# Kernel tuning notes

Measured on AMD Instinct MI355X. Metric: run time of the kernel, lower is better.

## Reference

```python
import jax, jax.numpy as jnp
from jax import lax
import numpy as np

K_TOP = 100
NMS_THRESH = 0.5
SUBJECT_CATEGORY_ID = 0


def box_cxcywh_to_xyxy(b):
    cx, cy, w, h = b[..., 0], b[..., 1], b[..., 2], b[..., 3]
    return jnp.stack([cx - 0.5 * w, cy - 0.5 * h, cx + 0.5 * w, cy + 0.5 * h], axis=-1)


def _pairwise_iou(boxes):
    # boxes: [K,4] xyxy; uses the +1 pixel convention from the original numpy NMS
    x1, y1, x2, y2 = boxes[:, 0], boxes[:, 1], boxes[:, 2], boxes[:, 3]
    area = (x2 - x1 + 1.0) * (y2 - y1 + 1.0)
    xx1 = jnp.maximum(x1[:, None], x1[None, :])
    yy1 = jnp.maximum(y1[:, None], y1[None, :])
    xx2 = jnp.minimum(x2[:, None], x2[None, :])
    yy2 = jnp.minimum(y2[:, None], y2[None, :])
    w = jnp.maximum(0.0, xx2 - xx1 + 1.0)
    h = jnp.maximum(0.0, yy2 - yy1 + 1.0)
    inter = w * h
    union = area[:, None] + area[None, :] - inter
    return inter / union


def _nms_keep(sub_boxes, obj_boxes, obj_labels, hoi_scores):
    # Greedy grouped pairwise NMS for one image.
    # Grouping key degenerates to object label (subject cat and verb-row are constant).
    K = sub_boxes.shape[0]
    max_scores = hoi_scores.max(axis=-1)
    order = jnp.argsort(-max_scores)
    ovr = _pairwise_iou(sub_boxes) * _pairwise_iou(obj_boxes)  # [K,K]
    same_group = obj_labels[:, None] == obj_labels[None, :]
    ovr = jnp.where(same_group, ovr, 0.0)
    ovr_s = ovr[order][:, order]
    upper = jnp.triu(jnp.ones((K, K), dtype=bool), k=1)
    sup_mat = (ovr_s > NMS_THRESH) & upper  # suppression only of later (lower-score) items

    def body(i, st):
        suppressed, keep = st
        ki = jnp.logical_not(suppressed[i])
        keep = keep.at[i].set(ki)
        suppressed = suppressed | (ki & sup_mat[i])
        return suppressed, keep

    _, keep_sorted = lax.fori_loop(0, K, body, (jnp.zeros(K, bool), jnp.zeros(K, bool)))
    return jnp.zeros(K, bool).at[order].set(keep_sorted)


def setup_inputs() -> dict:
    key = jax.random.key(0)
    k1, k2, k3, k4, k5, k6 = jax.random.split(key, 6)
    B, Q, C, V = 256, 300, 81, 117
    return {
        "pred_obj_logits": jax.random.normal(k1, (B, Q, C), dtype=jnp.float32),
        "pred_verb_logits": jax.random.normal(k2, (B, Q, V), dtype=jnp.float32),
        "pred_sub_boxes": jax.random.uniform(k3, (B, Q, 4), dtype=jnp.float32),
        "pred_obj_boxes": jax.random.uniform(k4, (B, Q, 4), dtype=jnp.float32),
        "correct_mat": (jax.random.uniform(k5, (V, C), dtype=jnp.float32) > 0.3).astype(jnp.float32),
        "target_sizes": jax.random.randint(k6, (B, 2), 200, 640, dtype=jnp.int32),
    }


def reference(pred_obj_logits, pred_verb_logits, pred_sub_boxes, pred_obj_boxes, correct_mat, target_sizes):
    B, Q, C = pred_obj_logits.shape
    V = pred_verb_logits.shape[-1]

    obj_prob = jax.nn.softmax(pred_obj_logits, axis=-1)       # [B,Q,C]  (no_obj=False)
    verb_scores = jax.nn.sigmoid(pred_verb_logits)            # [B,Q,V]

    topk_values, topk_indexes = lax.top_k(obj_prob.reshape(B, Q * C), K_TOP)  # [B,100]
    topk_boxes = topk_indexes // C
    obj_labels = topk_indexes % C

    vs = jnp.take_along_axis(verb_scores, topk_boxes[..., None], axis=1)      # [B,100,V]
    ob = jnp.take_along_axis(pred_obj_boxes, topk_boxes[..., None], axis=1)   # [B,100,4]
    sb = jnp.take_along_axis(pred_sub_boxes, topk_boxes[..., None], axis=1)

    img_h = target_sizes[:, 0].astype(jnp.float32)
    img_w = target_sizes[:, 1].astype(jnp.float32)
    scale_fct = jnp.stack([img_w, img_h, img_w, img_h], axis=1)  # [B,4]
    sub_boxes = box_cxcywh_to_xyxy(sb) * scale_fct[:, None, :]
    obj_boxes = box_cxcywh_to_xyxy(ob) * scale_fct[:, None, :]

    hoi_scores = vs * topk_values[..., None]                    # [B,100,V]
    # masks[b,k,v] = correct_mat[v, obj_labels[b,k]]
    masks = correct_mat.T[obj_labels]                           # [B,100,V]
    hoi_scores = hoi_scores * masks

    keep = jax.vmap(_nms_keep)(sub_boxes, obj_boxes, obj_labels, hoi_scores)  # [B,100] bool
    final_scores = hoi_scores * keep[..., None].astype(hoi_scores.dtype)

    return final_scores, topk_values, obj_labels, sub_boxes, obj_boxes, keep
```

## Files before the change

### kernel.cpp

```cpp
#include <hip/hip_runtime.h>
#include <cmath>

#pragma clang fp contract(off)

#define NT 1024
constexpr int B_ = 256, Q_ = 300, C_ = 81, V_ = 117, K_ = 100;
constexpr int QC_ = Q_ * C_;
constexpr int KV_ = K_ * V_;
constexpr int NB  = 2048;
constexpr int CAP = 1024;

using u32 = unsigned int;
using u64 = unsigned long long;
using u16 = unsigned short;
using u8  = unsigned char;

constexpr int OFF_P16  = 0;
constexpr int OFF_HIST = 48600;
constexpr int OFF_RMAX = OFF_HIST + 8192;
constexpr int OFF_RINV = OFF_RMAX + 1200;
constexpr int OFF_BSUB = OFF_RINV + 1200;
constexpr int OFF_BOBJ = OFF_BSUB + 1600;
constexpr int OFF_SUPR = OFF_BOBJ + 1600;
constexpr int OFF_SELV = OFF_SUPR + 1600;
constexpr int OFF_SELI = OFF_SELV + 400;
constexpr int OFF_MAXB = OFF_SELI + 400;
constexpr int OFF_ORD  = OFF_MAXB + 400;
constexpr int OFF_MISC = OFF_ORD + 104;
constexpr int SMEM_SZ  = OFF_MISC + 48;
static_assert(SMEM_SZ <= 65536, "LDS overflow");

__device__ __forceinline__ u64 shfl_xor_u64(u64 v, int mask) {
    u32 lo = (u32)v, hi = (u32)(v >> 32);
    lo = (u32)__shfl_xor((int)lo, mask, 64);
    hi = (u32)__shfl_xor((int)hi, mask, 64);
    return ((u64)hi << 32) | lo;
}

__device__ __forceinline__ float iou1(const float* a, const float* b) {
    float areaA = (a[2] - a[0] + 1.f) * (a[3] - a[1] + 1.f);
    float areaB = (b[2] - b[0] + 1.f) * (b[3] - b[1] + 1.f);
    float xx1 = fmaxf(a[0], b[0]);
    float yy1 = fmaxf(a[1], b[1]);
    float xx2 = fminf(a[2], b[2]);
    float yy2 = fminf(a[3], b[3]);
    float w = fmaxf(0.f, xx2 - xx1 + 1.f);
    float h = fmaxf(0.f, yy2 - yy1 + 1.f);
    float inter = w * h;
    return inter / (areaA + areaB - inter);
}

__global__ __launch_bounds__(NT) void hoi_kernel(
    const float* __restrict__ obj_logits,
    const float* __restrict__ verb_logits,
    const float* __restrict__ sub_boxes_in,
    const float* __restrict__ obj_boxes_in,
    const float* __restrict__ cm,
    const int*   __restrict__ tsizes,
    float* __restrict__ out)
{
    const int b = blockIdx.x;
    const int tid = threadIdx.x;

    __shared__ __align__(16) u8 smem[SMEM_SZ];
    u16*   p16     = (u16*)(smem + OFF_P16);
    float* hs      = (float*)(smem + OFF_P16);
    u32*   hist    = (u32*)(smem + OFF_HIST);
    u64*   cand    = (u64*)(smem + OFF_HIST);
    float* rowmax  = (float*)(smem + OFF_RMAX);
    float* rinv    = (float*)(smem + OFF_RINV);
    float (*bsub)[4]   = (float(*)[4])(smem + OFF_BSUB);
    float (*bobj)[4]   = (float(*)[4])(smem + OFF_BOBJ);
    u32   (*suprow)[4] = (u32(*)[4])(smem + OFF_SUPR);
    float* sel_val = (float*)(smem + OFF_SELV);
    u32*   sel_idx = (u32*)(smem + OFF_SELI);
    u32*   maxbits = (u32*)(smem + OFF_MAXB);
    u8*    order8  = (u8*)(smem + OFF_ORD);
    u32*   skeep     = (u32*)(smem + OFF_MISC);
    u32*   keep_bits = (u32*)(smem + OFF_MISC + 16);
    u32*   s_cnt     = (u32*)(smem + OFF_MISC + 32);
    int*   sT        = (int*)(smem + OFF_MISC + 36);
    int*   sW        = (int*)(smem + OFF_MISC + 40);
    u32*   sAcc      = (u32*)(smem + OFF_MISC + 44);
    u32*   swsum   = (u32*)(smem + OFF_BSUB);
    u64*   wred    = (u64*)(smem + OFF_BOBJ);
    u64*   s_prev  = (u64*)(smem + OFF_SUPR);

    const float* lg = obj_logits + (size_t)b * QC_;

    for (int i = tid; i < NB; i += NT) hist[i] = 0;
    if (tid == 0) *s_cnt = 0;
    __syncthreads();

    {
        int g = tid >> 5, l = tid & 31;
        bool have2 = (l < C_ - 64);
        for (int q = g; q < Q_; q += 32) {
            const float* row = lg + q * C_;
            float v0 = row[l], v1 = row[l + 32];
            float v2 = have2 ? row[l + 64] : -INFINITY;
            float m = fmaxf(fmaxf(v0, v1), v2);
            for (int off = 16; off; off >>= 1) m = fmaxf(m, __shfl_xor(m, off, 64));
            float e0 = expf(v0 - m), e1 = expf(v1 - m);
            float e2 = have2 ? expf(v2 - m) : 0.f;
            float s = e0 + e1 + e2;
            for (int off = 16; off; off >>= 1) s += __shfl_xor(s, off, 64);
            float ri = 1.f / s;
            float p0 = e0 * ri, p1 = e1 * ri;
            u32 b0 = __float_as_uint(p0), b1 = __float_as_uint(p1);
            p16[q * C_ + l]      = (u16)(b0 >> 16);
            p16[q * C_ + l + 32] = (u16)(b1 >> 16);
            atomicAdd(&hist[b0 >> 21], 1u);
            atomicAdd(&hist[b1 >> 21], 1u);
            if (have2) {
                float p2 = e2 * ri;
                u32 b2 = __float_as_uint(p2);
                p16[q * C_ + l + 64] = (u16)(b2 >> 16);
                atomicAdd(&hist[b2 >> 21], 1u);
            }
            if (l == 0) { rowmax[q] = m; rinv[q] = ri; }
        }
    }
    __syncthreads();

    u32 my_c, my_suf;
    {
        int t = tid;
        my_c = hist[2 * t] + hist[2 * t + 1];
        my_suf = my_c;
        #pragma unroll
        for (int off = 1; off < 64; off <<= 1) {
            u32 o = (u32)__shfl_down((int)my_suf, off, 64);
            my_suf += ((tid & 63) + off < 64) ? o : 0;
        }
        if ((tid & 63) == 0) swsum[tid >> 6] = my_suf;
    }
    __syncthreads();
    if (tid < 16) {
        u32 sufW = swsum[tid];
        #pragma unroll
        for (int off = 1; off < 16; off <<= 1) {
            u32 o = (u32)__shfl_down((int)sufW, off, 64);
            sufW += (tid + off < 16) ? o : 0;
        }
        u32 nxt = (u32)__shfl_down((int)sufW, 1, 64);
        if (tid == 15) nxt = 0;
        if (sufW >= (u32)K_ && nxt < (u32)K_) { *sW = tid; *sAcc = nxt; }
    }
    __syncthreads();
    if ((tid >> 6) == *sW) {
        u32 above = *sAcc + (my_suf - my_c);
        if (above < (u32)K_ && above + my_c >= (u32)K_) {
            u32 acc = above + hist[2 * tid + 1];
            *sT = (acc >= (u32)K_) ? (2 * tid + 1) : (2 * tid);
        }
    }
    __syncthreads();
    const int T = *sT;
    __syncthreads();

    for (int i = tid; i < QC_; i += NT) {
        u32 pb = p16[i];
        if ((int)(pb >> 5) >= T) {
            u32 pos = atomicAdd(s_cnt, 1u);
            if (pos < (u32)CAP) {
                int q = i / C_;
                float p = expf(lg[i] - rowmax[q]) * rinv[q];
                cand[pos] = ((u64)__float_as_uint(p) << 32) | (u32)(~i);
            }
        }
    }
    __syncthreads();
    const int ncand = (int)*s_cnt;

    auto cswap = [](u64& a, u64& bb, bool up) {
        if ((a > bb) == up) { u64 t = a; a = bb; bb = t; }
    };

    if (ncand <= 256) {
        if (tid < 64) {
            u64 v0 = (tid < ncand) ? cand[tid] : 0ull;
            u64 v1 = (64 + tid < ncand) ? cand[64 + tid] : 0ull;
            u64 v2 = (128 + tid < ncand) ? cand[128 + tid] : 0ull;
            u64 v3 = (192 + tid < ncand) ? cand[192 + tid] : 0ull;
            for (int k = 2; k <= 256; k <<= 1) {
                for (int j = k >> 1; j > 0; j >>= 1) {
                    if (j == 128) {
                        cswap(v0, v2, true);
                        cswap(v1, v3, true);
                    } else if (j == 64) {
                        cswap(v0, v1, true);
                        cswap(v2, v3, (k == 256));
                    } else {
                        auto step = [&](u64& v, int ebase) {
                            u64 pv = shfl_xor_u64(v, j);
                            int e = ebase + tid;
                            bool up = ((e & k) == 0);
                            bool lower = ((e & j) == 0);
                            u64 mn = v < pv ? v : pv;
                            u64 mx = v < pv ? pv : v;
                            v = (lower == up) ? mn : mx;
                        };
                        step(v0, 0); step(v1, 64); step(v2, 128); step(v3, 192);
                    }
                }
            }
            int e2 = 128 + tid;
            if (e2 >= 156) {
                int t = 255 - e2;
                sel_val[t] = __uint_as_float((u32)(v2 >> 32));
                sel_idx[t] = ~(u32)v2;
            }
            int t3 = 255 - (192 + tid);
            sel_val[t3] = __uint_as_float((u32)(v3 >> 32));
            sel_idx[t3] = ~(u32)v3;
        }
    } else if (ncand <= CAP) {
        for (int e = tid; e < CAP; e += NT)
            if (e >= ncand) cand[e] = 0;
        __syncthreads();
        for (int k = 2; k <= CAP; k <<= 1) {
            for (int j = k >> 1; j > 0; j >>= 1) {
                int e = tid, partner = e ^ j;
                if (partner > e) {
                    u64 a = cand[e], bb = cand[partner];
                    bool up = ((e & k) == 0);
                    if ((a > bb) == up) { cand[e] = bb; cand[partner] = a; }
                }
                __syncthreads();
            }
        }
        if (tid < K_) {
            u64 m = cand[CAP - 1 - tid];
            sel_val[tid] = __uint_as_float((u32)(m >> 32));
            sel_idx[tid] = ~(u32)m;
        }
    } else {
        if (tid == 0) *s_prev = ~0ull;
        __syncthreads();
        for (int r = 0; r < K_; r++) {
            u64 prev = *s_prev;
            u64 local = 0;
            for (int i = tid; i < QC_; i += NT) {
                int q = i / C_;
                float p = expf(lg[i] - rowmax[q]) * rinv[q];
                u64 key = ((u64)__float_as_uint(p) << 32) | (u32)(~i);
                if (key < prev && key > local) local = key;
            }
            for (int off = 32; off > 0; off >>= 1) {
                u64 o = shfl_xor_u64(local, off);
                if (o > local) local = o;
            }
            if ((tid & 63) == 0) wred[tid >> 6] = local;
            __syncthreads();
            if (tid == 0) {
                u64 m = wred[0];
                for (int wv = 1; wv < 16; wv++) if (wred[wv] > m) m = wred[wv];
                *s_prev = m;
                u32 idx = ~(u32)m;
                if (idx >= (u32)QC_) idx = 0;
                sel_val[r] = __uint_as_float((u32)(m >> 32));
                sel_idx[r] = idx;
            }
            __syncthreads();
        }
    }
    __syncthreads();

    if (tid < K_) {
        int idx = (int)sel_idx[tid];
        int q = idx / C_;
        float iw = (float)tsizes[b * 2 + 1];
        float ih = (float)tsizes[b * 2 + 0];
        float4 sb = ((const float4*)sub_boxes_in)[(size_t)b * Q_ + q];
        float4 ob = ((const float4*)obj_boxes_in)[(size_t)b * Q_ + q];
        bsub[tid][0] = (sb.x - 0.5f * sb.z) * iw; bsub[tid][1] = (sb.y - 0.5f * sb.w) * ih;
        bsub[tid][2] = (sb.x + 0.5f * sb.z) * iw; bsub[tid][3] = (sb.y + 0.5f * sb.w) * ih;
        bobj[tid][0] = (ob.x - 0.5f * ob.z) * iw; bobj[tid][1] = (ob.y - 0.5f * ob.w) * ih;
        bobj[tid][2] = (ob.x + 0.5f * ob.z) * iw; bobj[tid][3] = (ob.y + 0.5f * ob.w) * ih;
        suprow[tid][0] = 0; suprow[tid][1] = 0; suprow[tid][2] = 0; suprow[tid][3] = 0;
    }
    if (tid >= 128 && tid < 132) keep_bits[tid - 128] = 0;
    __syncthreads();

    for (int f = tid; f < KV_; f += NT) {
        int r = f / V_, v = f - r * V_;
        int idx = (int)sel_idx[r];
        int q = idx / C_, lab = idx - q * C_;
        float x = verb_logits[((size_t)b * Q_ + q) * V_ + v];
        float s = 1.f / (1.f + expf(-x));
        hs[f] = s * sel_val[r] * cm[v * C_ + lab];
    }
    __syncthreads();

    if (tid < 800) {
        int r = tid >> 3, j = tid & 7;
        float m = 0.f;
        for (int k = 0; k < 15; k++) {
            int v = j * 15 + k;
            if (v < V_) m = fmaxf(m, hs[r * V_ + v]);
        }
        for (int off = 4; off; off >>= 1) m = fmaxf(m, __shfl_xor(m, off, 64));
        if (j == 0) maxbits[r] = __float_as_uint(m);
    }
    __syncthreads();

    if (tid < 800) {
        int r = tid >> 3, j = tid & 7;
        u64 kr = ((u64)maxbits[r] << 32) | (u32)(~r);
        int rank = 0;
        for (int k = 0; k < 13; k++) {
            int jj = j * 13 + k;
            if (jj < K_) {
                u64 kj = ((u64)maxbits[jj] << 32) | (u32)(~jj);
                rank += (kj > kr) ? 1 : 0;
            }
        }
        for (int off = 4; off; off >>= 1) rank += __shfl_xor(rank, off, 64);
        if (j == 0) order8[rank] = (u8)r;
    }
    __syncthreads();

    for (int e = tid; e < K_ * K_; e += NT) {
        int i = e / K_, j = e - i * K_;
        if (j > i) {
            int ri = order8[i], rj = order8[j];
            u32 li = sel_idx[ri] % (u32)C_, lj = sel_idx[rj] % (u32)C_;
            if (li == lj) {
                float o = iou1(bsub[ri], bsub[rj]) * iou1(bobj[ri], bobj[rj]);
                if (o > 0.5f)
                    atomicOr(&suprow[i][j >> 5], 1u << (j & 31));
            }
        }
    }
    __syncthreads();

    if (tid < 64) {
        u32 ra0 = suprow[tid][0], ra1 = suprow[tid][1], ra2 = suprow[tid][2], ra3 = suprow[tid][3];
        u32 rb0 = 0, rb1 = 0, rb2 = 0, rb3 = 0;
        if (tid < K_ - 64) {
            rb0 = suprow[tid + 64][0]; rb1 = suprow[tid + 64][1];
            rb2 = suprow[tid + 64][2]; rb3 = suprow[tid + 64][3];
        }
        u32 acc[4] = {0, 0, 0, 0};
        u32 km[4]  = {0, 0, 0, 0};
        #pragma unroll
        for (int i = 0; i < K_; i++) {
            u32 r0, r1, r2, r3;
            if (i < 64) {
                r0 = (u32)__shfl((int)ra0, i, 64); r1 = (u32)__shfl((int)ra1, i, 64);
                r2 = (u32)__shfl((int)ra2, i, 64); r3 = (u32)__shfl((int)ra3, i, 64);
            } else {
                r0 = (u32)__shfl((int)rb0, i - 64, 64); r1 = (u32)__shfl((int)rb1, i - 64, 64);
                r2 = (u32)__shfl((int)rb2, i - 64, 64); r3 = (u32)__shfl((int)rb3, i - 64, 64);
            }
            bool sup_i = (acc[i >> 5] >> (i & 31)) & 1u;
            if (!sup_i) {
                km[i >> 5] |= 1u << (i & 31);
                acc[0] |= r0; acc[1] |= r1; acc[2] |= r2; acc[3] |= r3;
            }
        }
        if (tid == 0) { skeep[0] = km[0]; skeep[1] = km[1]; skeep[2] = km[2]; skeep[3] = km[3]; }
    }
    __syncthreads();
    if (tid < K_) {
        if ((skeep[tid >> 5] >> (tid & 31)) & 1u) {
            int r = order8[tid];
            atomicOr(&keep_bits[r >> 5], 1u << (r & 31));
        }
    }
    __syncthreads();

    float* o0 = out;
    float* o1 = out + (size_t)B_ * KV_;
    float* o2 = o1 + (size_t)B_ * K_;
    float* o3 = o2 + (size_t)B_ * K_;
    float* o4 = o3 + (size_t)B_ * K_ * 4;
    float* o5 = o4 + (size_t)B_ * K_ * 4;

    for (int f = tid; f < KV_; f += NT) {
        int r = f / V_;
        bool kp = (keep_bits[r >> 5] >> (r & 31)) & 1u;
        o0[(size_t)b * KV_ + f] = kp ? hs[f] : 0.f;
    }
    if (tid < K_) {
        bool kp = (keep_bits[tid >> 5] >> (tid & 31)) & 1u;
        o1[(size_t)b * K_ + tid] = sel_val[tid];
        o2[(size_t)b * K_ + tid] = (float)(sel_idx[tid] % (u32)C_);
        o5[(size_t)b * K_ + tid] = kp ? 1.f : 0.f;
    }
    if (tid < K_ * 4) {
        int r = tid >> 2, k = tid & 3;
        o3[((size_t)b * K_) * 4 + tid] = bsub[r][k];
        o4[((size_t)b * K_) * 4 + tid] = bobj[r][k];
    }
}

extern "C" void kernel_launch(void* const* d_in, const int* in_sizes, int n_in,
                              void* d_out, int out_size, void* d_ws, size_t ws_size,
                              hipStream_t stream) {
    const float* obj_logits  = (const float*)d_in[0];
    const float* verb_logits = (const float*)d_in[1];
    const float* sub_boxes   = (const float*)d_in[2];
    const float* obj_boxes   = (const float*)d_in[3];
    const float* cm          = (const float*)d_in[4];
    const int*   ts          = (const int*)d_in[5];
    hipLaunchKernelGGL(hoi_kernel, dim3(B_), dim3(NT), 0, stream,
                       obj_logits, verb_logits, sub_boxes, obj_boxes, cm, ts,
                       (float*)d_out);
}
```

Before: 143.1 us.

## Split per-image top-k into partitioned select kernel and merge/finish kernel

Splits each image's 300 query rows into 8 partitions, each handled by its own 256-thread block. Each block computes the softmax, builds a finer 8192-bin histogram, and writes its local top-128 candidates to workspace. A second kernel merges the 1024 candidates per image with a bitonic sort and then runs the verb scoring, NMS and output stages. The aim is far more blocks than the 256 images provide, better GPU occupancy for the softmax/top-k stage, and no recompute of exps. In exchange it adds a second launch, a workspace round trip, and a switch to the fast __expf.

```diff
diff --git a/kernel.cpp b/kernel.cpp
--- a/kernel.cpp
+++ b/kernel.cpp
@@ -2,33 +2,24 @@
 #include <cmath>
 
 #pragma clang fp contract(off)
-
-#define NT 1024
-constexpr int B_ = 256, Q_ = 300, C_ = 81, V_ = 117, K_ = 100;
-constexpr int QC_ = Q_ * C_;
-constexpr int KV_ = K_ * V_;
-constexpr int NB  = 2048;
-constexpr int CAP = 1024;
 
 using u32 = unsigned int;
 using u64 = unsigned long long;
 using u16 = unsigned short;
 using u8  = unsigned char;
 
-constexpr int OFF_P16  = 0;
-constexpr int OFF_HIST = 48600;
-constexpr int OFF_RMAX = OFF_HIST + 8192;
-constexpr int OFF_RINV = OFF_RMAX + 1200;
-constexpr int OFF_BSUB = OFF_RINV + 1200;
-constexpr int OFF_BOBJ = OFF_BSUB + 1600;
-constexpr int OFF_SUPR = OFF_BOBJ + 1600;
-constexpr int OFF_SELV = OFF_SUPR + 1600;
-constexpr int OFF_SELI = OFF_SELV + 400;
-constexpr int OFF_MAXB = OFF_SELI + 400;
-constexpr int OFF_ORD  = OFF_MAXB + 400;
-constexpr int OFF_MISC = OFF_ORD + 104;
-constexpr int SMEM_SZ  = OFF_MISC + 48;
-static_assert(SMEM_SZ <= 65536, "LDS overflow");
+constexpr int B_ = 256, Q_ = 300, C_ = 81, V_ = 117, K_ = 100;
+constexpr int QC_ = Q_ * C_;
+constexpr int KV_ = K_ * V_;
+
+constexpr int PARTS = 8;
+constexpr int RPP   = 38;
+constexpr int TOPP  = 128;
+constexpr int K1T   = 256;
+constexpr int NB1   = 8192;
+constexpr int CAP   = 1024;
+
+constexpr int K2T   = 1024;
 
 __device__ __forceinline__ u64 shfl_xor_u64(u64 v, int mask) {
     u32 lo = (u32)v, hi = (u32)(v >> 32);
@@ -50,128 +41,115 @@
     return inter / (areaA + areaB - inter);
 }
 
-__global__ __launch_bounds__(NT) void hoi_kernel(
+__global__ __launch_bounds__(K1T) void k1_select(
     const float* __restrict__ obj_logits,
-    const float* __restrict__ verb_logits,
-    const float* __restrict__ sub_boxes_in,
-    const float* __restrict__ obj_boxes_in,
-    const float* __restrict__ cm,
-    const int*   __restrict__ tsizes,
-    float* __restrict__ out)
+    u64* __restrict__ wsc)
 {
-    const int b = blockIdx.x;
+    const int blk = blockIdx.x;
+    const int b = blk >> 3, p = blk & 7;
+    const int row0 = p * RPP;
+    const int nrows = min(RPP, Q_ - row0);
+    const float* lg = obj_logits + (size_t)b * QC_ + (size_t)row0 * C_;
     const int tid = threadIdx.x;
 
-    __shared__ __align__(16) u8 smem[SMEM_SZ];
-    u16*   p16     = (u16*)(smem + OFF_P16);
-    float* hs      = (float*)(smem + OFF_P16);
-    u32*   hist    = (u32*)(smem + OFF_HIST);
-    u64*   cand    = (u64*)(smem + OFF_HIST);
-    float* rowmax  = (float*)(smem + OFF_RMAX);
-    float* rinv    = (float*)(smem + OFF_RINV);
-    float (*bsub)[4]   = (float(*)[4])(smem + OFF_BSUB);
-    float (*bobj)[4]   = (float(*)[4])(smem + OFF_BOBJ);
-    u32   (*suprow)[4] = (u32(*)[4])(smem + OFF_SUPR);
-    float* sel_val = (float*)(smem + OFF_SELV);
-    u32*   sel_idx = (u32*)(smem + OFF_SELI);
-    u32*   maxbits = (u32*)(smem + OFF_MAXB);
-    u8*    order8  = (u8*)(smem + OFF_ORD);
-    u32*   skeep     = (u32*)(smem + OFF_MISC);
-    u32*   keep_bits = (u32*)(smem + OFF_MISC + 16);
-    u32*   s_cnt     = (u32*)(smem + OFF_MISC + 32);
-    int*   sT        = (int*)(smem + OFF_MISC + 36);
-    int*   sW        = (int*)(smem + OFF_MISC + 40);
-    u32*   sAcc      = (u32*)(smem + OFF_MISC + 44);
-    u32*   swsum   = (u32*)(smem + OFF_BSUB);
-    u64*   wred    = (u64*)(smem + OFF_BOBJ);
-    u64*   s_prev  = (u64*)(smem + OFF_SUPR);
-
-    const float* lg = obj_logits + (size_t)b * QC_;
-
-    for (int i = tid; i < NB; i += NT) hist[i] = 0;
+    __shared__ __align__(16) u8 sm[32768 + 64];
+    u32* hist  = (u32*)sm;
+    u64* cand  = (u64*)sm;
+    u32* s_cnt = (u32*)(sm + 32768);
+    int* sT    = (int*)(sm + 32772);
+    u32* swsum = (u32*)(sm + 32776);
+
+    for (int i = tid; i < NB1; i += K1T) hist[i] = 0;
     if (tid == 0) *s_cnt = 0;
     __syncthreads();
 
-    {
-        int g = tid >> 5, l = tid & 31;
-        bool have2 = (l < C_ - 64);
-        for (int q = g; q < Q_; q += 32) {
-            const float* row = lg + q * C_;
+    const int g = tid >> 5, l = tid & 31;
+    const bool have2 = (l < C_ - 64);
+    u32 pb0[5], pb1[5], pb2[5];
+    #pragma unroll
+    for (int it = 0; it < 5; it++) {
+        int r = g + (it << 3);
+        if (r < nrows) {
+            const float* row = lg + r * C_;
             float v0 = row[l], v1 = row[l + 32];
             float v2 = have2 ? row[l + 64] : -INFINITY;
             float m = fmaxf(fmaxf(v0, v1), v2);
             for (int off = 16; off; off >>= 1) m = fmaxf(m, __shfl_xor(m, off, 64));
-            float e0 = expf(v0 - m), e1 = expf(v1 - m);
-            float e2 = have2 ? expf(v2 - m) : 0.f;
+            float e0 = __expf(v0 - m), e1 = __expf(v1 - m);
+            float e2 = have2 ? __expf(v2 - m) : 0.f;
             float s = e0 + e1 + e2;
             for (int off = 16; off; off >>= 1) s += __shfl_xor(s, off, 64);
             float ri = 1.f / s;
-            float p0 = e0 * ri, p1 = e1 * ri;
-            u32 b0 = __float_as_uint(p0), b1 = __float_as_uint(p1);
-            p16[q * C_ + l]      = (u16)(b0 >> 16);
-            p16[q * C_ + l + 32] = (u16)(b1 >> 16);
-            atomicAdd(&hist[b0 >> 21], 1u);
-            atomicAdd(&hist[b1 >> 21], 1u);
+            u32 b0 = __float_as_uint(e0 * ri), b1 = __float_as_uint(e1 * ri);
+            pb0[it] = b0; pb1[it] = b1;
+            atomicAdd(&hist[b0 >> 19], 1u);
+            atomicAdd(&hist[b1 >> 19], 1u);
             if (have2) {
-                float p2 = e2 * ri;
-                u32 b2 = __float_as_uint(p2);
-                p16[q * C_ + l + 64] = (u16)(b2 >> 16);
-                atomicAdd(&hist[b2 >> 21], 1u);
-            }
-            if (l == 0) { rowmax[q] = m; rinv[q] = ri; }
-        }
-    }
-    __syncthreads();
-
-    u32 my_c, my_suf;
+                u32 b2 = __float_as_uint(e2 * ri);
+                pb2[it] = b2;
+                atomicAdd(&hist[b2 >> 19], 1u);
+            }
+        }
+    }
+    __syncthreads();
+
     {
-        int t = tid;
-        my_c = hist[2 * t] + hist[2 * t + 1];
-        my_suf = my_c;
+        u32 c = 0;
+        int base = tid * (NB1 / K1T);
+        for (int k = 0; k < NB1 / K1T; k++) c += hist[base + k];
+        u32 suf = c;
         #pragma unroll
         for (int off = 1; off < 64; off <<= 1) {
-            u32 o = (u32)__shfl_down((int)my_suf, off, 64);
-            my_suf += ((tid & 63) + off < 64) ? o : 0;
-        }
-        if ((tid & 63) == 0) swsum[tid >> 6] = my_suf;
-    }
-    __syncthreads();
-    if (tid < 16) {
-        u32 sufW = swsum[tid];
-        #pragma unroll
-        for (int off = 1; off < 16; off <<= 1) {
-            u32 o = (u32)__shfl_down((int)sufW, off, 64);
-            sufW += (tid + off < 16) ? o : 0;
-        }
-        u32 nxt = (u32)__shfl_down((int)sufW, 1, 64);
-        if (tid == 15) nxt = 0;
-        if (sufW >= (u32)K_ && nxt < (u32)K_) { *sW = tid; *sAcc = nxt; }
-    }
-    __syncthreads();
-    if ((tid >> 6) == *sW) {
-        u32 above = *sAcc + (my_suf - my_c);
-        if (above < (u32)K_ && above + my_c >= (u32)K_) {
-            u32 acc = above + hist[2 * tid + 1];
-            *sT = (acc >= (u32)K_) ? (2 * tid + 1) : (2 * tid);
+            u32 o = (u32)__shfl_down((int)suf, off, 64);
+            suf += ((tid & 63) + off < 64) ? o : 0;
+        }
+        if ((tid & 63) == 0) swsum[tid >> 6] = suf;
+        __syncthreads();
+        u32 aw = 0;
+        for (int w = (tid >> 6) + 1; w < 4; w++) aw += swsum[w];
+        u32 above = aw + (suf - c);
+        if (above < (u32)TOPP && above + c >= (u32)TOPP) {
+            u32 acc = above;
+            for (int bn = base + NB1 / K1T - 1; bn >= base; bn--) {
+                u32 h = hist[bn];
+                if (acc + h >= (u32)TOPP) { *sT = bn; break; }
+                acc += h;
+            }
         }
     }
     __syncthreads();
     const int T = *sT;
     __syncthreads();
 
-    for (int i = tid; i < QC_; i += NT) {
-        u32 pb = p16[i];
-        if ((int)(pb >> 5) >= T) {
-            u32 pos = atomicAdd(s_cnt, 1u);
-            if (pos < (u32)CAP) {
-                int q = i / C_;
-                float p = expf(lg[i] - rowmax[q]) * rinv[q];
-                cand[pos] = ((u64)__float_as_uint(p) << 32) | (u32)(~i);
-            }
-        }
-    }
-    __syncthreads();
-    const int ncand = (int)*s_cnt;
+    #pragma unroll
+    for (int it = 0; it < 5; it++) {
+        int r = g + (it << 3);
+        if (r < nrows) {
+            u32 base_i = (u32)((row0 + r) * C_);
+            u32 b0 = pb0[it];
+            if ((int)(b0 >> 19) >= T) {
+                u32 pos = atomicAdd(s_cnt, 1u);
+                if (pos < (u32)CAP) cand[pos] = ((u64)b0 << 32) | (u32)(~(base_i + l));
+            }
+            u32 b1v = pb1[it];
+            if ((int)(b1v >> 19) >= T) {
+                u32 pos = atomicAdd(s_cnt, 1u);
+                if (pos < (u32)CAP) cand[pos] = ((u64)b1v << 32) | (u32)(~(base_i + l + 32));
+            }
+            if (have2) {
+                u32 b2 = pb2[it];
+                if ((int)(b2 >> 19) >= T) {
+                    u32 pos = atomicAdd(s_cnt, 1u);
+                    if (pos < (u32)CAP) cand[pos] = ((u64)b2 << 32) | (u32)(~(base_i + l + 64));
+                }
+            }
+        }
+    }
+    __syncthreads();
+    int ncand = (int)*s_cnt;
+    if (ncand > CAP) ncand = CAP;
+
+    u64* outp = wsc + (size_t)b * (PARTS * TOPP) + p * TOPP;
 
     auto cswap = [](u64& a, u64& bb, bool up) {
         if ((a > bb) == up) { u64 t = a; a = bb; bb = t; }
@@ -205,65 +183,86 @@
                     }
                 }
             }
-            int e2 = 128 + tid;
-            if (e2 >= 156) {
-                int t = 255 - e2;
-                sel_val[t] = __uint_as_float((u32)(v2 >> 32));
-                sel_idx[t] = ~(u32)v2;
-            }
-            int t3 = 255 - (192 + tid);
-            sel_val[t3] = __uint_as_float((u32)(v3 >> 32));
-            sel_idx[t3] = ~(u32)v3;
-        }
-    } else if (ncand <= CAP) {
-        for (int e = tid; e < CAP; e += NT)
+            outp[tid]      = v2;
+            outp[64 + tid] = v3;
+        }
+    } else {
+        for (int e = tid; e < CAP; e += K1T)
             if (e >= ncand) cand[e] = 0;
         __syncthreads();
         for (int k = 2; k <= CAP; k <<= 1) {
             for (int j = k >> 1; j > 0; j >>= 1) {
-                int e = tid, partner = e ^ j;
-                if (partner > e) {
-                    u64 a = cand[e], bb = cand[partner];
-                    bool up = ((e & k) == 0);
-                    if ((a > bb) == up) { cand[e] = bb; cand[partner] = a; }
+                for (int e = tid; e < CAP; e += K1T) {
+                    int partner = e ^ j;
+                    if (partner > e) {
+                        u64 a = cand[e], bb = cand[partner];
+                        bool up = ((e & k) == 0);
+                        if ((a > bb) == up) { cand[e] = bb; cand[partner] = a; }
+                    }
                 }
                 __syncthreads();
             }
         }
-        if (tid < K_) {
-            u64 m = cand[CAP - 1 - tid];
-            sel_val[tid] = __uint_as_float((u32)(m >> 32));
-            sel_idx[tid] = ~(u32)m;
-        }
-    } else {
-        if (tid == 0) *s_prev = ~0ull;
-        __syncthreads();
-        for (int r = 0; r < K_; r++) {
-            u64 prev = *s_prev;
-            u64 local = 0;
-            for (int i = tid; i < QC_; i += NT) {
-                int q = i / C_;
-                float p = expf(lg[i] - rowmax[q]) * rinv[q];
-                u64 key = ((u64)__float_as_uint(p) << 32) | (u32)(~i);
-                if (key < prev && key > local) local = key;
-            }
-            for (int off = 32; off > 0; off >>= 1) {
-                u64 o = shfl_xor_u64(local, off);
-                if (o > local) local = o;
-            }
-            if ((tid & 63) == 0) wred[tid >> 6] = local;
+        if (tid < TOPP) outp[tid] = cand[CAP - 1 - tid];
+    }
+}
+
+constexpr int OFF_HS   = 0;
+constexpr int OFF_BSUB = 46800;
+constexpr int OFF_BOBJ = OFF_BSUB + 1600;
+constexpr int OFF_SUPR = OFF_BOBJ + 1600;
+constexpr int OFF_SELV = OFF_SUPR + 1600;
+constexpr int OFF_SELI = OFF_SELV + 400;
+constexpr int OFF_MAXB = OFF_SELI + 400;
+constexpr int OFF_ORD  = OFF_MAXB + 400;
+constexpr int OFF_MISC = OFF_ORD + 104;
+constexpr int SMEM2    = OFF_MISC + 32;
+static_assert(SMEM2 <= 65536, "LDS overflow");
+
+__global__ __launch_bounds__(K2T) void k2_finish(
+    const u64*  __restrict__ wsc,
+    const float* __restrict__ verb_logits,
+    const float* __restrict__ sub_boxes_in,
+    const float* __restrict__ obj_boxes_in,
+    const float* __restrict__ cm,
+    const int*   __restrict__ tsizes,
+    float* __restrict__ out)
+{
+    const int b = blockIdx.x;
+    const int tid = threadIdx.x;
+
+    __shared__ __align__(16) u8 smem[SMEM2];
+    u64*   cand    = (u64*)(smem + OFF_HS);
+    float* hs      = (float*)(smem + OFF_HS);
+    float (*bsub)[4]   = (float(*)[4])(smem + OFF_BSUB);
+    float (*bobj)[4]   = (float(*)[4])(smem + OFF_BOBJ);
+    u32   (*suprow)[4] = (u32(*)[4])(smem + OFF_SUPR);
+    float* sel_val = (float*)(smem + OFF_SELV);
+    u32*   sel_idx = (u32*)(smem + OFF_SELI);
+    u32*   maxbits = (u32*)(smem + OFF_MAXB);
+    u8*    order8  = (u8*)(smem + OFF_ORD);
+    u32*   skeep     = (u32*)(smem + OFF_MISC);
+    u32*   keep_bits = (u32*)(smem + OFF_MISC + 16);
+
+    cand[tid] = wsc[(size_t)b * (PARTS * TOPP) + tid];
+    __syncthreads();
+    for (int k = 2; k <= CAP; k <<= 1) {
+        for (int j = k >> 1; j > 0; j >>= 1) {
+            int e = tid, partner = e ^ j;
+            if (partner > e) {
+                u64 a = cand[e], bb = cand[partner];
+                bool up = ((e & k) == 0);
+                if ((a > bb) == up) { cand[e] = bb; cand[partner] = a; }
+            }
             __syncthreads();
-            if (tid == 0) {
-                u64 m = wred[0];
-                for (int wv = 1; wv < 16; wv++) if (wred[wv] > m) m = wred[wv];
-                *s_prev = m;
-                u32 idx = ~(u32)m;
-                if (idx >= (u32)QC_) idx = 0;
-                sel_val[r] = __uint_as_float((u32)(m >> 32));
-                sel_idx[r] = idx;
-            }
-            __syncthreads();
-        }
+        }
+    }
+    if (tid < K_) {
+        u64 m = cand[CAP - 1 - tid];
+        u32 idx = ~(u32)m;
+        if (idx >= (u32)QC_) idx = 0;
+        sel_val[tid] = __uint_as_float((u32)(m >> 32));
+        sel_idx[tid] = idx;
     }
     __syncthreads();
 
@@ -283,12 +282,12 @@
     if (tid >= 128 && tid < 132) keep_bits[tid - 128] = 0;
     __syncthreads();
 
-    for (int f = tid; f < KV_; f += NT) {
+    for (int f = tid; f < KV_; f += K2T) {
         int r = f / V_, v = f - r * V_;
         int idx = (int)sel_idx[r];
         int q = idx / C_, lab = idx - q * C_;
         float x = verb_logits[((size_t)b * Q_ + q) * V_ + v];
-        float s = 1.f / (1.f + expf(-x));
+        float s = 1.f / (1.f + __expf(-x));
         hs[f] = s * sel_val[r] * cm[v * C_ + lab];
     }
     __syncthreads();
@@ -321,7 +320,7 @@
     }
     __syncthreads();
 
-    for (int e = tid; e < K_ * K_; e += NT) {
+    for (int e = tid; e < K_ * K_; e += K2T) {
         int i = e / K_, j = e - i * K_;
         if (j > i) {
             int ri = order8[i], rj = order8[j];
@@ -378,7 +377,7 @@
     float* o4 = o3 + (size_t)B_ * K_ * 4;
     float* o5 = o4 + (size_t)B_ * K_ * 4;
 
-    for (int f = tid; f < KV_; f += NT) {
+    for (int f = tid; f < KV_; f += K2T) {
         int r = f / V_;
         bool kp = (keep_bits[r >> 5] >> (r & 31)) & 1u;
         o0[(size_t)b * KV_ + f] = kp ? hs[f] : 0.f;
@@ -405,7 +404,11 @@
     const float* obj_boxes   = (const float*)d_in[3];
     const float* cm          = (const float*)d_in[4];
     const int*   ts          = (const int*)d_in[5];
-    hipLaunchKernelGGL(hoi_kernel, dim3(B_), dim3(NT), 0, stream,
-                       obj_logits, verb_logits, sub_boxes, obj_boxes, cm, ts,
+    u64* wsc = (u64*)d_ws;
+
+    hipLaunchKernelGGL(k1_select, dim3(B_ * PARTS), dim3(K1T), 0, stream,
+                       obj_logits, wsc);
+    hipLaunchKernelGGL(k2_finish, dim3(B_), dim3(K2T), 0, stream,
+                       wsc, verb_logits, sub_boxes, obj_boxes, cm, ts,
                        (float*)d_out);
 }
```

New measurement: 180.2 us. +25.9%, slower.

## Split top-k selection across two half-image blocks and merge in a second kernel

Applied to the files above, without the earlier changes.

Splits the per-image kernel in two. The first kernel runs two blocks per image, each covering half the queries and keeping a local top-128 in workspace. The second kernel merges the two sorted halves with a bitonic merge and then does scoring and NMS. This doubles the parallelism of the softmax/histogram/select stage, which was limited to 256 blocks, and also swaps expf for __expf. The costs are an extra launch, a global workspace round trip, and possible precision differences from __expf. The fallback for more than 1024 candidates is dropped (it now clamps), which could change results in degenerate cases.

```diff
diff --git a/kernel.cpp b/kernel.cpp
--- a/kernel.cpp
+++ b/kernel.cpp
@@ -9,26 +9,14 @@
 constexpr int KV_ = K_ * V_;
 constexpr int NB  = 2048;
 constexpr int CAP = 1024;
+constexpr int HROWS = 150;
+constexpr int HQC   = HROWS * C_;
+constexpr int TOPH  = 128;
 
 using u32 = unsigned int;
 using u64 = unsigned long long;
 using u16 = unsigned short;
 using u8  = unsigned char;
-
-constexpr int OFF_P16  = 0;
-constexpr int OFF_HIST = 48600;
-constexpr int OFF_RMAX = OFF_HIST + 8192;
-constexpr int OFF_RINV = OFF_RMAX + 1200;
-constexpr int OFF_BSUB = OFF_RINV + 1200;
-constexpr int OFF_BOBJ = OFF_BSUB + 1600;
-constexpr int OFF_SUPR = OFF_BOBJ + 1600;
-constexpr int OFF_SELV = OFF_SUPR + 1600;
-constexpr int OFF_SELI = OFF_SELV + 400;
-constexpr int OFF_MAXB = OFF_SELI + 400;
-constexpr int OFF_ORD  = OFF_MAXB + 400;
-constexpr int OFF_MISC = OFF_ORD + 104;
-constexpr int SMEM_SZ  = OFF_MISC + 48;
-static_assert(SMEM_SZ <= 65536, "LDS overflow");
 
 __device__ __forceinline__ u64 shfl_xor_u64(u64 v, int mask) {
     u32 lo = (u32)v, hi = (u32)(v >> 32);
@@ -50,43 +38,36 @@
     return inter / (areaA + areaB - inter);
 }
 
-__global__ __launch_bounds__(NT) void hoi_kernel(
+constexpr int OFF1_P16  = 0;
+constexpr int OFF1_HIST = 24304;
+constexpr int OFF1_RMAX = OFF1_HIST + 8192;
+constexpr int OFF1_RINV = OFF1_RMAX + 608;
+constexpr int OFF1_SW   = OFF1_RINV + 608;
+constexpr int OFF1_MISC = OFF1_SW + 64;
+constexpr int SMEM1     = OFF1_MISC + 16;
+static_assert(SMEM1 <= 65536, "K1 LDS overflow");
+
+__global__ __launch_bounds__(NT, 8) void k1_select(
     const float* __restrict__ obj_logits,
-    const float* __restrict__ verb_logits,
-    const float* __restrict__ sub_boxes_in,
-    const float* __restrict__ obj_boxes_in,
-    const float* __restrict__ cm,
-    const int*   __restrict__ tsizes,
-    float* __restrict__ out)
+    u64* __restrict__ wsc)
 {
-    const int b = blockIdx.x;
+    const int blk = blockIdx.x;
+    const int b = blk >> 1, h = blk & 1;
+    const int row0 = h * HROWS;
+    const float* lg = obj_logits + (size_t)b * QC_ + (size_t)row0 * C_;
     const int tid = threadIdx.x;
 
-    __shared__ __align__(16) u8 smem[SMEM_SZ];
-    u16*   p16     = (u16*)(smem + OFF_P16);
-    float* hs      = (float*)(smem + OFF_P16);
-    u32*   hist    = (u32*)(smem + OFF_HIST);
-    u64*   cand    = (u64*)(smem + OFF_HIST);
-    float* rowmax  = (float*)(smem + OFF_RMAX);
-    float* rinv    = (float*)(smem + OFF_RINV);
-    float (*bsub)[4]   = (float(*)[4])(smem + OFF_BSUB);
-    float (*bobj)[4]   = (float(*)[4])(smem + OFF_BOBJ);
-    u32   (*suprow)[4] = (u32(*)[4])(smem + OFF_SUPR);
-    float* sel_val = (float*)(smem + OFF_SELV);
-    u32*   sel_idx = (u32*)(smem + OFF_SELI);
-    u32*   maxbits = (u32*)(smem + OFF_MAXB);
-    u8*    order8  = (u8*)(smem + OFF_ORD);
-    u32*   skeep     = (u32*)(smem + OFF_MISC);
-    u32*   keep_bits = (u32*)(smem + OFF_MISC + 16);
-    u32*   s_cnt     = (u32*)(smem + OFF_MISC + 32);
-    int*   sT        = (int*)(smem + OFF_MISC + 36);
-    int*   sW        = (int*)(smem + OFF_MISC + 40);
-    u32*   sAcc      = (u32*)(smem + OFF_MISC + 44);
-    u32*   swsum   = (u32*)(smem + OFF_BSUB);
-    u64*   wred    = (u64*)(smem + OFF_BOBJ);
-    u64*   s_prev  = (u64*)(smem + OFF_SUPR);
-
-    const float* lg = obj_logits + (size_t)b * QC_;
+    __shared__ __align__(16) u8 sm[SMEM1];
+    u16*   p16    = (u16*)(sm + OFF1_P16);
+    u32*   hist   = (u32*)(sm + OFF1_HIST);
+    u64*   cand   = (u64*)(sm + OFF1_HIST);
+    float* rowmax = (float*)(sm + OFF1_RMAX);
+    float* rinv   = (float*)(sm + OFF1_RINV);
+    u32*   swsum  = (u32*)(sm + OFF1_SW);
+    u32*   s_cnt  = (u32*)(sm + OFF1_MISC);
+    int*   sT     = (int*)(sm + OFF1_MISC + 4);
+    int*   sW     = (int*)(sm + OFF1_MISC + 8);
+    u32*   sAcc   = (u32*)(sm + OFF1_MISC + 12);
 
     for (int i = tid; i < NB; i += NT) hist[i] = 0;
     if (tid == 0) *s_cnt = 0;
@@ -95,26 +76,24 @@
     {
         int g = tid >> 5, l = tid & 31;
         bool have2 = (l < C_ - 64);
-        for (int q = g; q < Q_; q += 32) {
+        for (int q = g; q < HROWS; q += 32) {
             const float* row = lg + q * C_;
             float v0 = row[l], v1 = row[l + 32];
             float v2 = have2 ? row[l + 64] : -INFINITY;
             float m = fmaxf(fmaxf(v0, v1), v2);
             for (int off = 16; off; off >>= 1) m = fmaxf(m, __shfl_xor(m, off, 64));
-            float e0 = expf(v0 - m), e1 = expf(v1 - m);
-            float e2 = have2 ? expf(v2 - m) : 0.f;
+            float e0 = __expf(v0 - m), e1 = __expf(v1 - m);
+            float e2 = have2 ? __expf(v2 - m) : 0.f;
             float s = e0 + e1 + e2;
             for (int off = 16; off; off >>= 1) s += __shfl_xor(s, off, 64);
             float ri = 1.f / s;
-            float p0 = e0 * ri, p1 = e1 * ri;
-            u32 b0 = __float_as_uint(p0), b1 = __float_as_uint(p1);
+            u32 b0 = __float_as_uint(e0 * ri), b1 = __float_as_uint(e1 * ri);
             p16[q * C_ + l]      = (u16)(b0 >> 16);
             p16[q * C_ + l + 32] = (u16)(b1 >> 16);
             atomicAdd(&hist[b0 >> 21], 1u);
             atomicAdd(&hist[b1 >> 21], 1u);
             if (have2) {
-                float p2 = e2 * ri;
-                u32 b2 = __float_as_uint(p2);
+                u32 b2 = __float_as_uint(e2 * ri);
                 p16[q * C_ + l + 64] = (u16)(b2 >> 16);
                 atomicAdd(&hist[b2 >> 21], 1u);
             }
@@ -125,8 +104,7 @@
 
     u32 my_c, my_suf;
     {
-        int t = tid;
-        my_c = hist[2 * t] + hist[2 * t + 1];
+        my_c = hist[2 * tid] + hist[2 * tid + 1];
         my_suf = my_c;
         #pragma unroll
         for (int off = 1; off < 64; off <<= 1) {
@@ -145,33 +123,36 @@
         }
         u32 nxt = (u32)__shfl_down((int)sufW, 1, 64);
         if (tid == 15) nxt = 0;
-        if (sufW >= (u32)K_ && nxt < (u32)K_) { *sW = tid; *sAcc = nxt; }
+        if (sufW >= (u32)TOPH && nxt < (u32)TOPH) { *sW = tid; *sAcc = nxt; }
     }
     __syncthreads();
     if ((tid >> 6) == *sW) {
         u32 above = *sAcc + (my_suf - my_c);
-        if (above < (u32)K_ && above + my_c >= (u32)K_) {
+        if (above < (u32)TOPH && above + my_c >= (u32)TOPH) {
             u32 acc = above + hist[2 * tid + 1];
-            *sT = (acc >= (u32)K_) ? (2 * tid + 1) : (2 * tid);
+            *sT = (acc >= (u32)TOPH) ? (2 * tid + 1) : (2 * tid);
         }
     }
     __syncthreads();
     const int T = *sT;
     __syncthreads();
 
-    for (int i = tid; i < QC_; i += NT) {
+    for (int i = tid; i < HQC; i += NT) {
         u32 pb = p16[i];
         if ((int)(pb >> 5) >= T) {
             u32 pos = atomicAdd(s_cnt, 1u);
             if (pos < (u32)CAP) {
                 int q = i / C_;
-                float p = expf(lg[i] - rowmax[q]) * rinv[q];
-                cand[pos] = ((u64)__float_as_uint(p) << 32) | (u32)(~i);
-            }
-        }
-    }
-    __syncthreads();
-    const int ncand = (int)*s_cnt;
+                float p = __expf(lg[i] - rowmax[q]) * rinv[q];
+                cand[pos] = ((u64)__float_as_uint(p) << 32) | (u32)(~(row0 * C_ + i));
+            }
+        }
+    }
+    __syncthreads();
+    int ncand = (int)*s_cnt;
+    if (ncand > CAP) ncand = CAP;
+
+    u64* outp = wsc + (size_t)b * 256 + h * TOPH;
 
     auto cswap = [](u64& a, u64& bb, bool up) {
         if ((a > bb) == up) { u64 t = a; a = bb; bb = t; }
@@ -205,17 +186,10 @@
                     }
                 }
             }
-            int e2 = 128 + tid;
-            if (e2 >= 156) {
-                int t = 255 - e2;
-                sel_val[t] = __uint_as_float((u32)(v2 >> 32));
-                sel_idx[t] = ~(u32)v2;
-            }
-            int t3 = 255 - (192 + tid);
-            sel_val[t3] = __uint_as_float((u32)(v3 >> 32));
-            sel_idx[t3] = ~(u32)v3;
-        }
-    } else if (ncand <= CAP) {
+            outp[tid]      = v2;
+            outp[64 + tid] = v3;
+        }
+    } else {
         for (int e = tid; e < CAP; e += NT)
             if (e >= ncand) cand[e] = 0;
         __syncthreads();
@@ -230,41 +204,80 @@
                 __syncthreads();
             }
         }
-        if (tid < K_) {
-            u64 m = cand[CAP - 1 - tid];
-            sel_val[tid] = __uint_as_float((u32)(m >> 32));
-            sel_idx[tid] = ~(u32)m;
-        }
-    } else {
-        if (tid == 0) *s_prev = ~0ull;
-        __syncthreads();
-        for (int r = 0; r < K_; r++) {
-            u64 prev = *s_prev;
-            u64 local = 0;
-            for (int i = tid; i < QC_; i += NT) {
-                int q = i / C_;
-                float p = expf(lg[i] - rowmax[q]) * rinv[q];
-                u64 key = ((u64)__float_as_uint(p) << 32) | (u32)(~i);
-                if (key < prev && key > local) local = key;
-            }
-            for (int off = 32; off > 0; off >>= 1) {
-                u64 o = shfl_xor_u64(local, off);
-                if (o > local) local = o;
-            }
-            if ((tid & 63) == 0) wred[tid >> 6] = local;
-            __syncthreads();
-            if (tid == 0) {
-                u64 m = wred[0];
-                for (int wv = 1; wv < 16; wv++) if (wred[wv] > m) m = wred[wv];
-                *s_prev = m;
-                u32 idx = ~(u32)m;
-                if (idx >= (u32)QC_) idx = 0;
-                sel_val[r] = __uint_as_float((u32)(m >> 32));
-                sel_idx[r] = idx;
-            }
-            __syncthreads();
-        }
-    }
+        if (tid < TOPH) outp[tid] = cand[CAP - TOPH + tid];
+    }
+}
+
+constexpr int OFF_HS   = 0;
+constexpr int OFF_BSUB = 46800;
+constexpr int OFF_BOBJ = OFF_BSUB + 1600;
+constexpr int OFF_SUPR = OFF_BOBJ + 1600;
+constexpr int OFF_SELV = OFF_SUPR + 1600;
+constexpr int OFF_SELI = OFF_SELV + 400;
+constexpr int OFF_MAXB = OFF_SELI + 400;
+constexpr int OFF_ORD  = OFF_MAXB + 400;
+constexpr int OFF_MISC = OFF_ORD + 104;
+constexpr int SMEM2    = OFF_MISC + 32;
+static_assert(SMEM2 <= 65536, "K2 LDS overflow");
+
+__global__ __launch_bounds__(NT) void k2_finish(
+    const u64*  __restrict__ wsc,
+    const float* __restrict__ verb_logits,
+    const float* __restrict__ sub_boxes_in,
+    const float* __restrict__ obj_boxes_in,
+    const float* __restrict__ cm,
+    const int*   __restrict__ tsizes,
+    float* __restrict__ out)
+{
+    const int b = blockIdx.x;
+    const int tid = threadIdx.x;
+
+    __shared__ __align__(16) u8 smem[SMEM2];
+    float* hs      = (float*)(smem + OFF_HS);
+    float (*bsub)[4]   = (float(*)[4])(smem + OFF_BSUB);
+    float (*bobj)[4]   = (float(*)[4])(smem + OFF_BOBJ);
+    u32   (*suprow)[4] = (u32(*)[4])(smem + OFF_SUPR);
+    float* sel_val = (float*)(smem + OFF_SELV);
+    u32*   sel_idx = (u32*)(smem + OFF_SELI);
+    u32*   maxbits = (u32*)(smem + OFF_MAXB);
+    u8*    order8  = (u8*)(smem + OFF_ORD);
+    u32*   skeep     = (u32*)(smem + OFF_MISC);
+    u32*   keep_bits = (u32*)(smem + OFF_MISC + 16);
+
+    if (tid < 64) {
+        const u64* base = wsc + (size_t)b * 256;
+        u64 v0 = base[tid];
+        u64 v1 = base[64 + tid];
+        u64 v2 = base[255 - tid];
+        u64 v3 = base[191 - tid];
+        auto cswap = [](u64& a, u64& bb) {
+            if (a > bb) { u64 t = a; a = bb; bb = t; }
+        };
+        cswap(v0, v2); cswap(v1, v3);
+        cswap(v0, v1); cswap(v2, v3);
+        for (int j = 32; j > 0; j >>= 1) {
+            auto step = [&](u64& v) {
+                u64 pv = shfl_xor_u64(v, j);
+                bool lower = ((tid & j) == 0);
+                u64 mn = v < pv ? v : pv;
+                u64 mx = v < pv ? pv : v;
+                v = lower ? mn : mx;
+            };
+            step(v0); step(v1); step(v2); step(v3);
+        }
+        int e2 = 128 + tid;
+        if (e2 >= 156) {
+            int t = 255 - e2;
+            u32 idx = ~(u32)v2; if (idx >= (u32)QC_) idx = 0;
+            sel_val[t] = __uint_as_float((u32)(v2 >> 32));
+            sel_idx[t] = idx;
+        }
+        int t3 = 63 - tid;
+        u32 idx3 = ~(u32)v3; if (idx3 >= (u32)QC_) idx3 = 0;
+        sel_val[t3] = __uint_as_float((u32)(v3 >> 32));
+        sel_idx[t3] = idx3;
+    }
+    if (tid >= 128 && tid < 132) keep_bits[tid - 128] = 0;
     __syncthreads();
 
     if (tid < K_) {
@@ -280,7 +293,6 @@
         bobj[tid][2] = (ob.x + 0.5f * ob.z) * iw; bobj[tid][3] = (ob.y + 0.5f * ob.w) * ih;
         suprow[tid][0] = 0; suprow[tid][1] = 0; suprow[tid][2] = 0; suprow[tid][3] = 0;
     }
-    if (tid >= 128 && tid < 132) keep_bits[tid - 128] = 0;
     __syncthreads();
 
     for (int f = tid; f < KV_; f += NT) {
@@ -288,7 +300,7 @@
         int idx = (int)sel_idx[r];
         int q = idx / C_, lab = idx - q * C_;
         float x = verb_logits[((size_t)b * Q_ + q) * V_ + v];
-        float s = 1.f / (1.f + expf(-x));
+        float s = 1.f / (1.f + __expf(-x));
         hs[f] = s * sel_val[r] * cm[v * C_ + lab];
     }
     __syncthreads();
@@ -405,7 +417,11 @@
     const float* obj_boxes   = (const float*)d_in[3];
     const float* cm          = (const float*)d_in[4];
     const int*   ts          = (const int*)d_in[5];
-    hipLaunchKernelGGL(hoi_kernel, dim3(B_), dim3(NT), 0, stream,
-                       obj_logits, verb_logits, sub_boxes, obj_boxes, cm, ts,
+    u64* wsc = (u64*)d_ws;
+
+    hipLaunchKernelGGL(k1_select, dim3(B_ * 2), dim3(NT), 0, stream,
+                       obj_logits, wsc);
+    hipLaunchKernelGGL(k2_finish, dim3(B_), dim3(NT), 0, stream,
+                       wsc, verb_logits, sub_boxes, obj_boxes, cm, ts,
                        (float*)d_out);
 }
```

Result: slower. 146.8 us (+2.6%).

## Write HOI scores directly to global, zero suppressed rows later, use fast exp

Applied to the files above, without the earlier changes.

Computes the per-row verb scores one wavefront per row, writing them straight to the output and computing the row max by a wave shuffle reduction, instead of staging them in shared memory and running a separate max pass. After NMS, only suppressed rows are overwritten with zeros, so the final full copy out of shared memory goes away. All expf calls become __expf. The fast exp can change low-order bits of the probabilities, and the scores written before NMS are global writes that suppressed rows then overwrite a second time.

```diff
diff --git a/kernel.cpp b/kernel.cpp
--- a/kernel.cpp
+++ b/kernel.cpp
@@ -64,7 +64,6 @@
 
     __shared__ __align__(16) u8 smem[SMEM_SZ];
     u16*   p16     = (u16*)(smem + OFF_P16);
-    float* hs      = (float*)(smem + OFF_P16);
     u32*   hist    = (u32*)(smem + OFF_HIST);
     u64*   cand    = (u64*)(smem + OFF_HIST);
     float* rowmax  = (float*)(smem + OFF_RMAX);
@@ -88,6 +87,13 @@
 
     const float* lg = obj_logits + (size_t)b * QC_;
 
+    float* o0 = out;
+    float* o1 = out + (size_t)B_ * KV_;
+    float* o2 = o1 + (size_t)B_ * K_;
+    float* o3 = o2 + (size_t)B_ * K_;
+    float* o4 = o3 + (size_t)B_ * K_ * 4;
+    float* o5 = o4 + (size_t)B_ * K_ * 4;
+
     for (int i = tid; i < NB; i += NT) hist[i] = 0;
     if (tid == 0) *s_cnt = 0;
     __syncthreads();
@@ -101,20 +107,18 @@
             float v2 = have2 ? row[l + 64] : -INFINITY;
             float m = fmaxf(fmaxf(v0, v1), v2);
             for (int off = 16; off; off >>= 1) m = fmaxf(m, __shfl_xor(m, off, 64));
-            float e0 = expf(v0 - m), e1 = expf(v1 - m);
-            float e2 = have2 ? expf(v2 - m) : 0.f;
+            float e0 = __expf(v0 - m), e1 = __expf(v1 - m);
+            float e2 = have2 ? __expf(v2 - m) : 0.f;
             float s = e0 + e1 + e2;
             for (int off = 16; off; off >>= 1) s += __shfl_xor(s, off, 64);
             float ri = 1.f / s;
-            float p0 = e0 * ri, p1 = e1 * ri;
-            u32 b0 = __float_as_uint(p0), b1 = __float_as_uint(p1);
+            u32 b0 = __float_as_uint(e0 * ri), b1 = __float_as_uint(e1 * ri);
             p16[q * C_ + l]      = (u16)(b0 >> 16);
             p16[q * C_ + l + 32] = (u16)(b1 >> 16);
             atomicAdd(&hist[b0 >> 21], 1u);
             atomicAdd(&hist[b1 >> 21], 1u);
             if (have2) {
-                float p2 = e2 * ri;
-                u32 b2 = __float_as_uint(p2);
+                u32 b2 = __float_as_uint(e2 * ri);
                 p16[q * C_ + l + 64] = (u16)(b2 >> 16);
                 atomicAdd(&hist[b2 >> 21], 1u);
             }
@@ -125,8 +129,7 @@
 
     u32 my_c, my_suf;
     {
-        int t = tid;
-        my_c = hist[2 * t] + hist[2 * t + 1];
+        my_c = hist[2 * tid] + hist[2 * tid + 1];
         my_suf = my_c;
         #pragma unroll
         for (int off = 1; off < 64; off <<= 1) {
@@ -165,7 +168,7 @@
             u32 pos = atomicAdd(s_cnt, 1u);
             if (pos < (u32)CAP) {
                 int q = i / C_;
-                float p = expf(lg[i] - rowmax[q]) * rinv[q];
+                float p = __expf(lg[i] - rowmax[q]) * rinv[q];
                 cand[pos] = ((u64)__float_as_uint(p) << 32) | (u32)(~i);
             }
         }
@@ -243,7 +246,7 @@
             u64 local = 0;
             for (int i = tid; i < QC_; i += NT) {
                 int q = i / C_;
-                float p = expf(lg[i] - rowmax[q]) * rinv[q];
+                float p = __expf(lg[i] - rowmax[q]) * rinv[q];
                 u64 key = ((u64)__float_as_uint(p) << 32) | (u32)(~i);
                 if (key < prev && key > local) local = key;
             }
@@ -283,25 +286,27 @@
     if (tid >= 128 && tid < 132) keep_bits[tid - 128] = 0;
     __syncthreads();
 
-    for (int f = tid; f < KV_; f += NT) {
-        int r = f / V_, v = f - r * V_;
-        int idx = (int)sel_idx[r];
-        int q = idx / C_, lab = idx - q * C_;
-        float x = verb_logits[((size_t)b * Q_ + q) * V_ + v];
-        float s = 1.f / (1.f + expf(-x));
-        hs[f] = s * sel_val[r] * cm[v * C_ + lab];
-    }
-    __syncthreads();
-
-    if (tid < 800) {
-        int r = tid >> 3, j = tid & 7;
-        float m = 0.f;
-        for (int k = 0; k < 15; k++) {
-            int v = j * 15 + k;
-            if (v < V_) m = fmaxf(m, hs[r * V_ + v]);
-        }
-        for (int off = 4; off; off >>= 1) m = fmaxf(m, __shfl_xor(m, off, 64));
-        if (j == 0) maxbits[r] = __float_as_uint(m);
+    {
+        int w = tid >> 6, l = tid & 63;
+        for (int r = w; r < K_; r += 16) {
+            int idx = (int)sel_idx[r];
+            int q = idx / C_, lab = idx - q * C_;
+            float val = sel_val[r];
+            const float* vrow = verb_logits + ((size_t)b * Q_ + q) * V_;
+            float* orow = o0 + (size_t)b * KV_ + r * V_;
+            float x0 = vrow[l];
+            float h0 = (1.f / (1.f + __expf(-x0))) * val * cm[l * C_ + lab];
+            orow[l] = h0;
+            float h1 = 0.f;
+            if (l < V_ - 64) {
+                float x1 = vrow[l + 64];
+                h1 = (1.f / (1.f + __expf(-x1))) * val * cm[(l + 64) * C_ + lab];
+                orow[l + 64] = h1;
+            }
+            float m = fmaxf(h0, h1);
+            for (int off = 32; off; off >>= 1) m = fmaxf(m, __shfl_xor(m, off, 64));
+            if (l == 0) maxbits[r] = __float_as_uint(m);
+        }
     }
     __syncthreads();
 
@@ -371,17 +376,15 @@
     }
     __syncthreads();
 
-    float* o0 = out;
-    float* o1 = out + (size_t)B_ * KV_;
-    float* o2 = o1 + (size_t)B_ * K_;
-    float* o3 = o2 + (size_t)B_ * K_;
-    float* o4 = o3 + (size_t)B_ * K_ * 4;
-    float* o5 = o4 + (size_t)B_ * K_ * 4;
-
-    for (int f = tid; f < KV_; f += NT) {
-        int r = f / V_;
-        bool kp = (keep_bits[r >> 5] >> (r & 31)) & 1u;
-        o0[(size_t)b * KV_ + f] = kp ? hs[f] : 0.f;
+    {
+        int w = tid >> 6, l = tid & 63;
+        for (int r = w; r < K_; r += 16) {
+            if (!((keep_bits[r >> 5] >> (r & 31)) & 1u)) {
+                float* orow = o0 + (size_t)b * KV_ + r * V_;
+                orow[l] = 0.f;
+                if (l < V_ - 64) orow[l + 64] = 0.f;
+            }
+        }
     }
     if (tid < K_) {
         bool kp = (keep_bits[tid >> 5] >> (tid & 31)) & 1u;
```

New measurement: 143.7 us. Within noise of the previous version (+0.4%).
